# Kernel tuning notes

Hardware: AMD Instinct MI355X
Metric: run time of the kernel (lower is better)

## Reference

```python
import jax, jax.numpy as jnp
import numpy as np

B, L, H, S = 64, 1024, 768, 32
NH, HD = 8, H // 8
SEP = 102
EPS_LN = 1e-5


def setup_inputs() -> dict:
    key = jax.random.key(0)
    ks = jax.random.split(key, 16)
    # input_ids with exactly S SEP tokens per row at positions (j+1)*(L//S)-1
    ids = jax.random.randint(ks[0], (B, L), 1000, 30000, dtype=jnp.int64)
    sep_idx = (jnp.arange(1, S + 1) * (L // S)) - 1  # [S]
    ids = ids.at[:, sep_idx].set(SEP)
    attention_mask = jnp.ones((B, L), dtype=jnp.int32)
    labels = jax.random.randint(ks[1], (B, S), 0, 2, dtype=jnp.int64)
    sequence_output = jax.random.normal(ks[2], (B, L, H), dtype=jnp.float32)
    sc = 0.02
    params = dict(
        enc_W=jax.random.normal(ks[3], (H, H), jnp.float32) * sc,
        enc_b=jnp.zeros((H,), jnp.float32),
        enc_ln_g=jnp.ones((H,), jnp.float32),
        enc_ln_b=jnp.zeros((H,), jnp.float32),
        in_proj_W=jax.random.normal(ks[4], (3 * H, H), jnp.float32) * sc,
        in_proj_b=jnp.zeros((3 * H,), jnp.float32),
        out_proj_W=jax.random.normal(ks[5], (H, H), jnp.float32) * sc,
        out_proj_b=jnp.zeros((H,), jnp.float32),
        cls_W1=jax.random.normal(ks[6], (H, H), jnp.float32) * sc,
        cls_b1=jnp.zeros((H,), jnp.float32),
        cls_ln_g=jnp.ones((H,), jnp.float32),
        cls_ln_b=jnp.zeros((H,), jnp.float32),
        cls_W2=jax.random.normal(ks[7], (2, H), jnp.float32) * sc,
        cls_b2=jnp.zeros((2,), jnp.float32),
    )
    return dict(input_ids=ids, attention_mask=attention_mask, labels=labels,
                sequence_output=sequence_output, **params)


def _layernorm(x, g, b):
    m = jnp.mean(x, axis=-1, keepdims=True)
    v = jnp.mean((x - m) ** 2, axis=-1, keepdims=True)
    return (x - m) * jax.lax.rsqrt(v + EPS_LN) * g + b


def _gelu(x):
    return jax.nn.gelu(x, approximate=False)


def reference(input_ids, attention_mask, labels, sequence_output,
              enc_W, enc_b, enc_ln_g, enc_ln_b,
              in_proj_W, in_proj_b, out_proj_W, out_proj_b,
              cls_W1, cls_b1, cls_ln_g, cls_ln_b, cls_W2, cls_b2):
    # sep positions per sample (exactly S per row by construction)
    sep_pos = jax.vmap(lambda r: jnp.nonzero(r == SEP, size=S, fill_value=L - 1)[0])(input_ids)  # [B,S]
    all_pos = jnp.concatenate([jnp.zeros((B, 1), sep_pos.dtype), sep_pos], axis=1)  # [B,S+1]
    starts, ends = all_pos[:, :S], all_pos[:, 1:]  # inclusive [start, end] as in slice start:end+1
    t = jnp.arange(L)
    seg = (t[None, None, :] >= starts[:, :, None]) & (t[None, None, :] <= ends[:, :, None])  # [B,S,L]
    m = seg.astype(jnp.float32) * attention_mask[:, None, :].astype(jnp.float32)
    denom = jnp.sum(m, axis=-1, keepdims=True) + 1e-10  # [B,S,1]
    reps = jnp.einsum('bsl,bld->bsd', m, sequence_output) / denom  # segment mean pool
    # sentence encoder: Linear -> LN -> (dropout off) -> GELU
    x = _gelu(_layernorm(reps @ enc_W.T + enc_b, enc_ln_g, enc_ln_b))  # [B,S,H]
    # per-sample MHA (self-attention over sentences), dropout off
    qkv = x @ in_proj_W.T + in_proj_b  # [B,S,3H]
    q, k, v = jnp.split(qkv, 3, axis=-1)
    def heads(z):
        return z.reshape(B, S, NH, HD).transpose(0, 2, 1, 3)  # [B,NH,S,HD]
    q, k, v = heads(q), heads(k), heads(v)
    scores = jnp.einsum('bhqd,bhkd->bhqk', q, k) / jnp.sqrt(jnp.float32(HD))
    attn = jax.nn.softmax(scores, axis=-1)
    o = jnp.einsum('bhqk,bhkd->bhqd', attn, v).transpose(0, 2, 1, 3).reshape(B, S, H)
    attended = o @ out_proj_W.T + out_proj_b
    # classifier
    h = _gelu(_layernorm(attended @ cls_W1.T + cls_b1, cls_ln_g, cls_ln_b))
    logits = h @ cls_W2.T + cls_b2  # [B,S,2] (current_sentences == max_sentences, no padding)
    # cross entropy with ignore_index=-100
    flat_logits = logits.reshape(-1, 2)
    flat_labels = labels.reshape(-1)
    valid = flat_labels != -100
    safe = jnp.where(valid, flat_labels, 0)
    logp = jax.nn.log_softmax(flat_logits, axis=-1)
    nll = -jnp.take_along_axis(logp, safe[:, None], axis=-1)[:, 0]
    loss = jnp.sum(jnp.where(valid, nll, 0.0)) / jnp.maximum(jnp.sum(valid), 1)
    return loss, logits
```

## Files before the change

kernel.cpp:

```cpp
#include <hip/hip_runtime.h>
#include <math.h>

#define Bdim 64
#define Ldim 1024
#define Hdim 768
#define Sdim 32
#define NHdim 8
#define HDdim 96
#define SEP_ID 102

typedef unsigned short ushort_t;
typedef __attribute__((ext_vector_type(8))) short bf16x8;
typedef __attribute__((ext_vector_type(4))) float f32x4;

__device__ __forceinline__ ushort_t f2b(float f) {
    unsigned u = __builtin_bit_cast(unsigned, f);
    u += 0x7fffu + ((u >> 16) & 1u);
    return (ushort_t)(u >> 16);
}
__device__ __forceinline__ float b2f(ushort_t v) {
    unsigned u = ((unsigned)v) << 16;
    return __builtin_bit_cast(float, u);
}

__global__ __launch_bounds__(1024) void prep_kernel(const int* __restrict__ ids,
                                                    int* __restrict__ sep_pos,
                                                    const float* __restrict__ w0,
                                                    const float* __restrict__ w1,
                                                    const float* __restrict__ w2,
                                                    const float* __restrict__ w3,
                                                    ushort_t* __restrict__ dst) {
    __shared__ unsigned long long masks[16];
    int blk = blockIdx.x;
    int t = threadIdx.x;
    if (blk < 64) {
        unsigned long long m = __ballot(ids[(size_t)blk * Ldim + t] == SEP_ID);
        if ((t & 63) == 0) masks[t >> 6] = m;
        __syncthreads();
        if (t == 0) {
            int cnt = 0;
            for (int w = 0; w < 16 && cnt < Sdim; ++w) {
                unsigned long long mk = masks[w];
                while (mk && cnt < Sdim) {
                    int bit = __ffsll((unsigned long long)mk) - 1;
                    sep_pos[blk * Sdim + cnt++] = w * 64 + bit;
                    mk &= mk - 1;
                }
            }
            for (; cnt < Sdim; ++cnt) sep_pos[blk * Sdim + cnt] = Ldim - 1;
        }
    } else {
        int idx = (blk - 64) * 1024 + t;
        const float* src; int off;
        if (idx < 147456)      { src = w0; off = idx; }
        else if (idx < 589824) { src = w1; off = idx - 147456; }
        else if (idx < 737280) { src = w2; off = idx - 589824; }
        else                   { src = w3; off = idx - 737280; }
        float4 v = ((const float4*)src)[off];
        ushort4 ov; ov.x = f2b(v.x); ov.y = f2b(v.y); ov.z = f2b(v.z); ov.w = f2b(v.w);
        ((ushort4*)dst)[idx] = ov;
    }
}

__global__ __launch_bounds__(192) void pool_kernel(const float* __restrict__ seq,
                                                   const int* __restrict__ sep_pos,
                                                   const int* __restrict__ amask,
                                                   ushort_t* __restrict__ reps) {
    int bs = blockIdx.x;
    int b = bs >> 5, s = bs & 31;
    int start = (s == 0) ? 0 : sep_pos[b * Sdim + s - 1];
    int end = sep_pos[b * Sdim + s];
    int t = threadIdx.x;
    const float* base = seq + (size_t)b * Ldim * Hdim;
    const int* am = amask + b * Ldim;
    float4 A0 = {0,0,0,0}, A1 = {0,0,0,0}, A2 = {0,0,0,0}, A3 = {0,0,0,0};
    float d0 = 0.f, d1 = 0.f, d2 = 0.f, d3 = 0.f;
    int l = start;
    for (; l + 3 <= end; l += 4) {
        float m0 = (float)am[l],     m1 = (float)am[l + 1];
        float m2 = (float)am[l + 2], m3 = (float)am[l + 3];
        float4 v0 = ((const float4*)(base + (size_t)l * Hdim))[t];
        float4 v1 = ((const float4*)(base + (size_t)(l + 1) * Hdim))[t];
        float4 v2 = ((const float4*)(base + (size_t)(l + 2) * Hdim))[t];
        float4 v3 = ((const float4*)(base + (size_t)(l + 3) * Hdim))[t];
        d0 += m0; d1 += m1; d2 += m2; d3 += m3;
        A0.x += m0 * v0.x; A0.y += m0 * v0.y; A0.z += m0 * v0.z; A0.w += m0 * v0.w;
        A1.x += m1 * v1.x; A1.y += m1 * v1.y; A1.z += m1 * v1.z; A1.w += m1 * v1.w;
        A2.x += m2 * v2.x; A2.y += m2 * v2.y; A2.z += m2 * v2.z; A2.w += m2 * v2.w;
        A3.x += m3 * v3.x; A3.y += m3 * v3.y; A3.z += m3 * v3.z; A3.w += m3 * v3.w;
    }
    for (; l <= end; ++l) {
        float m0 = (float)am[l];
        float4 v0 = ((const float4*)(base + (size_t)l * Hdim))[t];
        d0 += m0;
        A0.x += m0 * v0.x; A0.y += m0 * v0.y; A0.z += m0 * v0.z; A0.w += m0 * v0.w;
    }
    float denom = d0 + d1 + d2 + d3;
    float inv = 1.f / (denom + 1e-10f);
    float4 acc;
    acc.x = (A0.x + A1.x + A2.x + A3.x) * inv;
    acc.y = (A0.y + A1.y + A2.y + A3.y) * inv;
    acc.z = (A0.z + A1.z + A2.z + A3.z) * inv;
    acc.w = (A0.w + A1.w + A2.w + A3.w) * inv;
    ushort4 o;
    o.x = f2b(acc.x); o.y = f2b(acc.y); o.z = f2b(acc.z); o.w = f2b(acc.w);
    ((ushort4*)(reps + (size_t)bs * Hdim))[t] = o;
}

__global__ __launch_bounds__(256) void gemm_mfma(const ushort_t* __restrict__ A,
                                                 const ushort_t* __restrict__ W,
                                                 const float* __restrict__ bias,
                                                 ushort_t* __restrict__ Cout,
                                                 int M, int N, int K) {
    __shared__ __attribute__((aligned(16))) ushort_t Al[2][64][64];
    __shared__ __attribute__((aligned(16))) ushort_t Bl[2][64][64];
    int tid = threadIdx.x;
    int wid = tid >> 6, lane = tid & 63;
    int rowBase = blockIdx.x * 64, colBase = blockIdx.y * 64;
    int wm = (wid >> 1) * 32, wn = (wid & 1) * 32;

    int srow = lane >> 3;
    int sblk = (lane & 7) ^ srow;
    const ushort_t* Abase = A + (size_t)(rowBase + wid * 16 + srow) * K + sblk * 8;
    const ushort_t* Wbase = W + (size_t)(colBase + wid * 16 + srow) * K + sblk * 8;

    f32x4 acc[2][2] = {};

#define STAGE(bufi, kofs)                                                                    \
    do {                                                                                     \
        const ushort_t* ag = Abase + (kofs);                                                 \
        const ushort_t* wg = Wbase + (kofs);                                                 \
        __builtin_amdgcn_global_load_lds(ag,           &Al[bufi][wid * 16][0],     16, 0, 0); \
        __builtin_amdgcn_global_load_lds(ag + 8 * K,   &Al[bufi][wid * 16 + 8][0], 16, 0, 0); \
        __builtin_amdgcn_global_load_lds(wg,           &Bl[bufi][wid * 16][0],     16, 0, 0); \
        __builtin_amdgcn_global_load_lds(wg + 8 * K,   &Bl[bufi][wid * 16 + 8][0], 16, 0, 0); \
    } while (0)

    STAGE(0, 0);
    __syncthreads();
    int nk = K >> 6;
    int lr = lane & 15;
    int lxor = lane & 7;
    for (int t = 0; t < nk; ++t) {
        if (t + 1 < nk) STAGE((t + 1) & 1, (t + 1) * 64);
        int cb = t & 1;
#pragma unroll
        for (int ks = 0; ks < 2; ++ks) {
            int pblk = ((ks * 4 + (lane >> 4)) ^ lxor) * 8;
            bf16x8 af[2], wf[2];
            af[0] = *(const bf16x8*)&Al[cb][wm + lr][pblk];
            af[1] = *(const bf16x8*)&Al[cb][wm + 16 + lr][pblk];
            wf[0] = *(const bf16x8*)&Bl[cb][wn + lr][pblk];
            wf[1] = *(const bf16x8*)&Bl[cb][wn + 16 + lr][pblk];
#pragma unroll
            for (int i = 0; i < 2; ++i)
#pragma unroll
                for (int j = 0; j < 2; ++j)
                    acc[i][j] = __builtin_amdgcn_mfma_f32_16x16x32_bf16(af[i], wf[j], acc[i][j], 0, 0, 0);
        }
        __syncthreads();
    }
#undef STAGE

    int lrow = (lane >> 4) * 4, lcol = lane & 15;
#pragma unroll
    for (int ni = 0; ni < 2; ++ni) {
        int c = colBase + wn + ni * 16 + lcol;
        float bv = bias[c];
#pragma unroll
        for (int mi = 0; mi < 2; ++mi) {
            int rb = rowBase + wm + mi * 16 + lrow;
#pragma unroll
            for (int j = 0; j < 4; ++j)
                Cout[(size_t)(rb + j) * N + c] = f2b(acc[mi][ni][j] + bv);
        }
    }
}

__global__ __launch_bounds__(192) void ln_gelu(const ushort_t* __restrict__ X,
                                               const float* __restrict__ g,
                                               const float* __restrict__ bt,
                                               ushort_t* __restrict__ Y) {
    int row = blockIdx.x;
    int t = threadIdx.x;
    ushort4 v = ((const ushort4*)(X + (size_t)row * Hdim))[t];
    float vals[4] = { b2f(v.x), b2f(v.y), b2f(v.z), b2f(v.w) };
    float s = vals[0] + vals[1] + vals[2] + vals[3];
    float s2 = vals[0]*vals[0] + vals[1]*vals[1] + vals[2]*vals[2] + vals[3]*vals[3];
#pragma unroll
    for (int off = 32; off; off >>= 1) { s += __shfl_down(s, off); s2 += __shfl_down(s2, off); }
    __shared__ float red[6];
    int wid = t >> 6;
    if ((t & 63) == 0) { red[wid * 2] = s; red[wid * 2 + 1] = s2; }
    __syncthreads();
    s  = red[0] + red[2] + red[4];
    s2 = red[1] + red[3] + red[5];
    float mean = s / Hdim;
    float var  = s2 / Hdim - mean * mean;
    float rstd = rsqrtf(var + 1e-5f);
    float4 gv = ((const float4*)g)[t];
    float4 bv = ((const float4*)bt)[t];
    float gg[4] = { gv.x, gv.y, gv.z, gv.w };
    float bb[4] = { bv.x, bv.y, bv.z, bv.w };
    ushort4 o;
    ushort_t* op = (ushort_t*)&o;
#pragma unroll
    for (int i = 0; i < 4; ++i) {
        float xn = (vals[i] - mean) * rstd * gg[i] + bb[i];
        float ge = 0.5f * xn * (1.f + erff(xn * 0.70710678118654752f));
        op[i] = f2b(ge);
    }
    ((ushort4*)(Y + (size_t)row * Hdim))[t] = o;
}

__global__ __launch_bounds__(256) void attn_kernel(const ushort_t* __restrict__ qkv,
                                                   ushort_t* __restrict__ o) {
    int bh = blockIdx.x;
    int b = bh >> 3, h = bh & 7;
    __shared__ float qs[Sdim][100], ks_[Sdim][100], vs[Sdim][100];
    __shared__ float sc[Sdim][33];
    int tid = threadIdx.x;
    for (int idx = tid; idx < 2304; idx += 256) {
        int m = idx / 768;
        int w = idx - m * 768;
        int s = w / 24, d4 = (w - s * 24) * 4;
        ushort4 v = *(const ushort4*)(qkv + (size_t)(b * Sdim + s) * (3 * Hdim) + m * Hdim + h * HDdim + d4);
        float* dst = (m == 0 ? &qs[s][d4] : (m == 1 ? &ks_[s][d4] : &vs[s][d4]));
        dst[0] = b2f(v.x); dst[1] = b2f(v.y); dst[2] = b2f(v.z); dst[3] = b2f(v.w);
    }
    __syncthreads();
    int ti = tid >> 4, tj = tid & 15;
    float a00 = 0.f, a01 = 0.f, a10 = 0.f, a11 = 0.f;
#pragma unroll 6
    for (int d = 0; d < HDdim; d += 4) {
        float4 q0 = *(const float4*)&qs[ti][d];
        float4 q1 = *(const float4*)&qs[ti + 16][d];
        float4 k0 = *(const float4*)&ks_[tj][d];
        float4 k1 = *(const float4*)&ks_[tj + 16][d];
        a00 += q0.x*k0.x + q0.y*k0.y + q0.z*k0.z + q0.w*k0.w;
        a01 += q0.x*k1.x + q0.y*k1.y + q0.z*k1.z + q0.w*k1.w;
        a10 += q1.x*k0.x + q1.y*k0.y + q1.z*k0.z + q1.w*k0.w;
        a11 += q1.x*k1.x + q1.y*k1.y + q1.z*k1.z + q1.w*k1.w;
    }
    const float sscale = 0.102062072615966f;
    sc[ti][tj]           = a00 * sscale;
    sc[ti][tj + 16]      = a01 * sscale;
    sc[ti + 16][tj]      = a10 * sscale;
    sc[ti + 16][tj + 16] = a11 * sscale;
    __syncthreads();
    int row = tid >> 3, jg = tid & 7;
    float v0 = sc[row][jg], v1 = sc[row][jg + 8], v2 = sc[row][jg + 16], v3 = sc[row][jg + 24];
    float mx = fmaxf(fmaxf(v0, v1), fmaxf(v2, v3));
#pragma unroll
    for (int m = 1; m <= 4; m <<= 1) mx = fmaxf(mx, __shfl_xor(mx, m));
    v0 = expf(v0 - mx); v1 = expf(v1 - mx); v2 = expf(v2 - mx); v3 = expf(v3 - mx);
    float sum = v0 + v1 + v2 + v3;
#pragma unroll
    for (int m = 1; m <= 4; m <<= 1) sum += __shfl_xor(sum, m);
    float inv = 1.f / sum;
    sc[row][jg] = v0 * inv; sc[row][jg + 8] = v1 * inv;
    sc[row][jg + 16] = v2 * inv; sc[row][jg + 24] = v3 * inv;
    __syncthreads();
    for (int idx = tid; idx < 768; idx += 256) {
        int ii = idx / 24, d4 = (idx - ii * 24) * 4;
        float o0 = 0.f, o1 = 0.f, o2 = 0.f, o3 = 0.f;
#pragma unroll 8
        for (int j = 0; j < Sdim; ++j) {
            float p = sc[ii][j];
            float4 vv = *(const float4*)&vs[j][d4];
            o0 += p * vv.x; o1 += p * vv.y; o2 += p * vv.z; o3 += p * vv.w;
        }
        ushort4 ov; ov.x = f2b(o0); ov.y = f2b(o1); ov.z = f2b(o2); ov.w = f2b(o3);
        *(ushort4*)(o + (size_t)(b * Sdim + ii) * Hdim + h * HDdim + d4) = ov;
    }
}

__global__ __launch_bounds__(192) void logits_kernel(const ushort_t* __restrict__ Hh,
                                                     const float* __restrict__ W2,
                                                     const float* __restrict__ b2,
                                                     float* __restrict__ out) {
    int row = blockIdx.x;
    int t = threadIdx.x;
    ushort4 hv = ((const ushort4*)(Hh + (size_t)row * Hdim))[t];
    float4 w0 = ((const float4*)W2)[t];
    float4 w1 = ((const float4*)(W2 + Hdim))[t];
    float h0 = b2f(hv.x), h1 = b2f(hv.y), h2 = b2f(hv.z), h3 = b2f(hv.w);
    float a0 = h0 * w0.x + h1 * w0.y + h2 * w0.z + h3 * w0.w;
    float a1 = h0 * w1.x + h1 * w1.y + h2 * w1.z + h3 * w1.w;
#pragma unroll
    for (int off = 32; off; off >>= 1) { a0 += __shfl_down(a0, off); a1 += __shfl_down(a1, off); }
    __shared__ float red[6];
    int wid = t >> 6;
    if ((t & 63) == 0) { red[wid * 2] = a0; red[wid * 2 + 1] = a1; }
    __syncthreads();
    if (t == 0) {
        out[row * 2 + 0] = red[0] + red[2] + red[4] + b2[0];
        out[row * 2 + 1] = red[1] + red[3] + red[5] + b2[1];
    }
}

__global__ __launch_bounds__(256) void loss_kernel(const float* __restrict__ logits,
                                                   const int* __restrict__ labels,
                                                   float* __restrict__ out) {
    int t = threadIdx.x;
    float sum = 0.f, cnt = 0.f;
    for (int i = t; i < Bdim * Sdim; i += 256) {
        int lab = labels[i];
        if (lab != -100) {
            float l0 = logits[i * 2], l1 = logits[i * 2 + 1];
            float mx = fmaxf(l0, l1);
            float lse = mx + logf(expf(l0 - mx) + expf(l1 - mx));
            sum += lse - (lab ? l1 : l0);
            cnt += 1.f;
        }
    }
#pragma unroll
    for (int off = 32; off; off >>= 1) { sum += __shfl_down(sum, off); cnt += __shfl_down(cnt, off); }
    __shared__ float red[8];
    int wid = t >> 6;
    if ((t & 63) == 0) { red[wid * 2] = sum; red[wid * 2 + 1] = cnt; }
    __syncthreads();
    if (t == 0) {
        float ts = red[0] + red[2] + red[4] + red[6];
        float tc = red[1] + red[3] + red[5] + red[7];
        out[0] = ts / fmaxf(tc, 1.f);
    }
}

extern "C" void kernel_launch(void* const* d_in, const int* in_sizes, int n_in,
                              void* d_out, int out_size, void* d_ws, size_t ws_size,
                              hipStream_t stream) {
    const int*   input_ids  = (const int*)d_in[0];
    const int*   amask      = (const int*)d_in[1];
    const int*   labels     = (const int*)d_in[2];
    const float* seq        = (const float*)d_in[3];
    const float* enc_W      = (const float*)d_in[4];
    const float* enc_b      = (const float*)d_in[5];
    const float* enc_ln_g   = (const float*)d_in[6];
    const float* enc_ln_b   = (const float*)d_in[7];
    const float* in_proj_W  = (const float*)d_in[8];
    const float* in_proj_b  = (const float*)d_in[9];
    const float* out_proj_W = (const float*)d_in[10];
    const float* out_proj_b = (const float*)d_in[11];
    const float* cls_W1     = (const float*)d_in[12];
    const float* cls_b1     = (const float*)d_in[13];
    const float* cls_ln_g   = (const float*)d_in[14];
    const float* cls_ln_b   = (const float*)d_in[15];
    const float* cls_W2     = (const float*)d_in[16];
    const float* cls_b2     = (const float*)d_in[17];

    float* out = (float*)d_out;

    char* ws = (char*)d_ws;
    const size_t MS = (size_t)Bdim * Sdim;
    int*      sep_pos = (int*)ws;
    ushort_t* wbf     = (ushort_t*)(ws + 8192);
    ushort_t* bf_a    = (ushort_t*)(ws + 8192 + 7077888);
    ushort_t* bf_b    = bf_a + MS * Hdim;
    ushort_t* bf_c    = bf_b + MS * Hdim;
    ushort_t* bf_d    = bf_c + MS * Hdim;
    ushort_t* bf_qkv  = bf_d + MS * Hdim;

    ushort_t* encWb     = wbf;
    ushort_t* inprojWb  = wbf + 589824;
    ushort_t* outprojWb = wbf + 2359296;
    ushort_t* clsW1b    = wbf + 2949120;

    prep_kernel<<<928, 1024, 0, stream>>>(input_ids, sep_pos,
                                          enc_W, in_proj_W, out_proj_W, cls_W1, wbf);
    pool_kernel<<<Bdim * Sdim, 192, 0, stream>>>(seq, sep_pos, amask, bf_a);
    { dim3 g(32, 12); gemm_mfma<<<g, 256, 0, stream>>>(bf_a, encWb, enc_b, bf_d, (int)MS, Hdim, Hdim); }
    ln_gelu<<<Bdim * Sdim, 192, 0, stream>>>(bf_d, enc_ln_g, enc_ln_b, bf_b);
    { dim3 g(32, 36); gemm_mfma<<<g, 256, 0, stream>>>(bf_b, inprojWb, in_proj_b, bf_qkv, (int)MS, 3 * Hdim, Hdim); }
    attn_kernel<<<Bdim * NHdim, 256, 0, stream>>>(bf_qkv, bf_c);
    { dim3 g(32, 12); gemm_mfma<<<g, 256, 0, stream>>>(bf_c, outprojWb, out_proj_b, bf_a, (int)MS, Hdim, Hdim); }
    { dim3 g(32, 12); gemm_mfma<<<g, 256, 0, stream>>>(bf_a, clsW1b, cls_b1, bf_d, (int)MS, Hdim, Hdim); }
    ln_gelu<<<Bdim * Sdim, 192, 0, stream>>>(bf_d, cls_ln_g, cls_ln_b, bf_b);
    logits_kernel<<<Bdim * Sdim, 192, 0, stream>>>(bf_b, cls_W2, cls_b2, out + 1);
    loss_kernel<<<1, 256, 0, stream>>>(out + 1, labels, out);
}
```

Measured before the change: 120.8 us.

## Fuse SEP scan into pooling kernel and fuse classifier LN-GELU into logits

Merges the prep and pool kernels: each pooling block recomputes its own SEP positions from a ballot scan of its row, and the weight bf16 conversion blocks share the same launch. Separately, fuses the final layernorm+GELU with the 2-way logits projection, so the intermediate bf16 activation is no longer written and re-read. This removes two launches and a global sep_pos round trip. The cost is redundant SEP scanning (32 blocks per row) and a one-pass variance formula with slightly different numerics.

```diff
diff --git a/kernel.cpp b/kernel.cpp
--- a/kernel.cpp
+++ b/kernel.cpp
@@ -23,34 +23,19 @@
     return __builtin_bit_cast(float, u);
 }
 
-__global__ __launch_bounds__(1024) void prep_kernel(const int* __restrict__ ids,
-                                                    int* __restrict__ sep_pos,
-                                                    const float* __restrict__ w0,
-                                                    const float* __restrict__ w1,
-                                                    const float* __restrict__ w2,
-                                                    const float* __restrict__ w3,
-                                                    ushort_t* __restrict__ dst) {
-    __shared__ unsigned long long masks[16];
+__global__ __launch_bounds__(192) void prep_pool_kernel(const float* __restrict__ seq,
+                                                        const int* __restrict__ ids,
+                                                        const int* __restrict__ amask,
+                                                        const float* __restrict__ w0,
+                                                        const float* __restrict__ w1,
+                                                        const float* __restrict__ w2,
+                                                        const float* __restrict__ w3,
+                                                        ushort_t* __restrict__ wdst,
+                                                        ushort_t* __restrict__ reps) {
     int blk = blockIdx.x;
     int t = threadIdx.x;
-    if (blk < 64) {
-        unsigned long long m = __ballot(ids[(size_t)blk * Ldim + t] == SEP_ID);
-        if ((t & 63) == 0) masks[t >> 6] = m;
-        __syncthreads();
-        if (t == 0) {
-            int cnt = 0;
-            for (int w = 0; w < 16 && cnt < Sdim; ++w) {
-                unsigned long long mk = masks[w];
-                while (mk && cnt < Sdim) {
-                    int bit = __ffsll((unsigned long long)mk) - 1;
-                    sep_pos[blk * Sdim + cnt++] = w * 64 + bit;
-                    mk &= mk - 1;
-                }
-            }
-            for (; cnt < Sdim; ++cnt) sep_pos[blk * Sdim + cnt] = Ldim - 1;
-        }
-    } else {
-        int idx = (blk - 64) * 1024 + t;
+    if (blk >= 2048) {
+        int idx = (blk - 2048) * 192 + t;
         const float* src; int off;
         if (idx < 147456)      { src = w0; off = idx; }
         else if (idx < 589824) { src = w1; off = idx - 147456; }
@@ -58,19 +43,46 @@
         else                   { src = w3; off = idx - 737280; }
         float4 v = ((const float4*)src)[off];
         ushort4 ov; ov.x = f2b(v.x); ov.y = f2b(v.y); ov.z = f2b(v.z); ov.w = f2b(v.w);
-        ((ushort4*)dst)[idx] = ov;
-    }
-}
-
-__global__ __launch_bounds__(192) void pool_kernel(const float* __restrict__ seq,
-                                                   const int* __restrict__ sep_pos,
-                                                   const int* __restrict__ amask,
-                                                   ushort_t* __restrict__ reps) {
-    int bs = blockIdx.x;
-    int b = bs >> 5, s = bs & 31;
-    int start = (s == 0) ? 0 : sep_pos[b * Sdim + s - 1];
-    int end = sep_pos[b * Sdim + s];
-    int t = threadIdx.x;
+        ((ushort4*)wdst)[idx] = ov;
+        return;
+    }
+    int b = blk >> 5, s = blk & 31;
+    __shared__ unsigned long long masks[18];
+    const int* idrow = ids + (size_t)b * Ldim;
+    int wv = t >> 6, ln = t & 63;
+#pragma unroll
+    for (int r = 0; r < 6; ++r) {
+        int p = r * 192 + t;
+        bool is = (p < Ldim) && (idrow[p] == SEP_ID);
+        unsigned long long m = __ballot(is);
+        if (ln == 0) masks[r * 3 + wv] = m;
+    }
+    __syncthreads();
+    int start, end;
+    {
+        int need0 = s - 1, need1 = s;
+        int p0 = Ldim - 1, p1 = Ldim - 1;
+        int cnt = 0;
+#pragma unroll
+        for (int i = 0; i < 18; ++i) {
+            unsigned long long mk = masks[i];
+            int pc = __popcll(mk);
+            int base = (i / 3) * 192 + (i % 3) * 64;
+            if (need0 >= cnt && need0 < cnt + pc) {
+                unsigned long long mm = mk;
+                for (int j = cnt; j < need0; ++j) mm &= mm - 1;
+                p0 = base + __ffsll(mm) - 1;
+            }
+            if (need1 >= cnt && need1 < cnt + pc) {
+                unsigned long long mm = mk;
+                for (int j = cnt; j < need1; ++j) mm &= mm - 1;
+                p1 = base + __ffsll(mm) - 1;
+            }
+            cnt += pc;
+        }
+        start = (s == 0) ? 0 : p0;
+        end = p1;
+    }
     const float* base = seq + (size_t)b * Ldim * Hdim;
     const int* am = amask + b * Ldim;
     float4 A0 = {0,0,0,0}, A1 = {0,0,0,0}, A2 = {0,0,0,0}, A3 = {0,0,0,0};
@@ -104,7 +116,7 @@
     acc.w = (A0.w + A1.w + A2.w + A3.w) * inv;
     ushort4 o;
     o.x = f2b(acc.x); o.y = f2b(acc.y); o.z = f2b(acc.z); o.w = f2b(acc.w);
-    ((ushort4*)(reps + (size_t)bs * Hdim))[t] = o;
+    ((ushort4*)(reps + (size_t)blk * Hdim))[t] = o;
 }
 
 __global__ __launch_bounds__(256) void gemm_mfma(const ushort_t* __restrict__ A,
@@ -275,27 +287,52 @@
     }
 }
 
-__global__ __launch_bounds__(192) void logits_kernel(const ushort_t* __restrict__ Hh,
-                                                     const float* __restrict__ W2,
-                                                     const float* __restrict__ b2,
-                                                     float* __restrict__ out) {
+__global__ __launch_bounds__(192) void cls_head_kernel(const ushort_t* __restrict__ X,
+                                                       const float* __restrict__ g,
+                                                       const float* __restrict__ bt,
+                                                       const float* __restrict__ W2,
+                                                       const float* __restrict__ b2,
+                                                       float* __restrict__ out) {
     int row = blockIdx.x;
     int t = threadIdx.x;
-    ushort4 hv = ((const ushort4*)(Hh + (size_t)row * Hdim))[t];
+    ushort4 v = ((const ushort4*)(X + (size_t)row * Hdim))[t];
+    float vals[4] = { b2f(v.x), b2f(v.y), b2f(v.z), b2f(v.w) };
+    float s = vals[0] + vals[1] + vals[2] + vals[3];
+    float s2 = vals[0]*vals[0] + vals[1]*vals[1] + vals[2]*vals[2] + vals[3]*vals[3];
+#pragma unroll
+    for (int off = 32; off; off >>= 1) { s += __shfl_down(s, off); s2 += __shfl_down(s2, off); }
+    __shared__ float red1[6], red2[6];
+    int wid = t >> 6;
+    if ((t & 63) == 0) { red1[wid * 2] = s; red1[wid * 2 + 1] = s2; }
+    __syncthreads();
+    s  = red1[0] + red1[2] + red1[4];
+    s2 = red1[1] + red1[3] + red1[5];
+    float mean = s / Hdim;
+    float var  = s2 / Hdim - mean * mean;
+    float rstd = rsqrtf(var + 1e-5f);
+    float4 gv = ((const float4*)g)[t];
+    float4 bv = ((const float4*)bt)[t];
     float4 w0 = ((const float4*)W2)[t];
     float4 w1 = ((const float4*)(W2 + Hdim))[t];
-    float h0 = b2f(hv.x), h1 = b2f(hv.y), h2 = b2f(hv.z), h3 = b2f(hv.w);
-    float a0 = h0 * w0.x + h1 * w0.y + h2 * w0.z + h3 * w0.w;
-    float a1 = h0 * w1.x + h1 * w1.y + h2 * w1.z + h3 * w1.w;
+    float gg[4] = { gv.x, gv.y, gv.z, gv.w };
+    float bb[4] = { bv.x, bv.y, bv.z, bv.w };
+    float ww0[4] = { w0.x, w0.y, w0.z, w0.w };
+    float ww1[4] = { w1.x, w1.y, w1.z, w1.w };
+    float a0 = 0.f, a1 = 0.f;
+#pragma unroll
+    for (int i = 0; i < 4; ++i) {
+        float xn = (vals[i] - mean) * rstd * gg[i] + bb[i];
+        float ge = 0.5f * xn * (1.f + erff(xn * 0.70710678118654752f));
+        a0 += ge * ww0[i];
+        a1 += ge * ww1[i];
+    }
 #pragma unroll
     for (int off = 32; off; off >>= 1) { a0 += __shfl_down(a0, off); a1 += __shfl_down(a1, off); }
-    __shared__ float red[6];
-    int wid = t >> 6;
-    if ((t & 63) == 0) { red[wid * 2] = a0; red[wid * 2 + 1] = a1; }
+    if ((t & 63) == 0) { red2[wid * 2] = a0; red2[wid * 2 + 1] = a1; }
     __syncthreads();
     if (t == 0) {
-        out[row * 2 + 0] = red[0] + red[2] + red[4] + b2[0];
-        out[row * 2 + 1] = red[1] + red[3] + red[5] + b2[1];
+        out[row * 2 + 0] = red2[0] + red2[2] + red2[4] + b2[0];
+        out[row * 2 + 1] = red2[1] + red2[3] + red2[5] + b2[1];
     }
 }
 
@@ -353,9 +390,8 @@
 
     char* ws = (char*)d_ws;
     const size_t MS = (size_t)Bdim * Sdim;
-    int*      sep_pos = (int*)ws;
-    ushort_t* wbf     = (ushort_t*)(ws + 8192);
-    ushort_t* bf_a    = (ushort_t*)(ws + 8192 + 7077888);
+    ushort_t* wbf     = (ushort_t*)(ws);
+    ushort_t* bf_a    = (ushort_t*)(ws + 7077888);
     ushort_t* bf_b    = bf_a + MS * Hdim;
     ushort_t* bf_c    = bf_b + MS * Hdim;
     ushort_t* bf_d    = bf_c + MS * Hdim;
@@ -366,16 +402,15 @@
     ushort_t* outprojWb = wbf + 2359296;
     ushort_t* clsW1b    = wbf + 2949120;
 
-    prep_kernel<<<928, 1024, 0, stream>>>(input_ids, sep_pos,
-                                          enc_W, in_proj_W, out_proj_W, cls_W1, wbf);
-    pool_kernel<<<Bdim * Sdim, 192, 0, stream>>>(seq, sep_pos, amask, bf_a);
+    prep_pool_kernel<<<6656, 192, 0, stream>>>(seq, input_ids, amask,
+                                               enc_W, in_proj_W, out_proj_W, cls_W1,
+                                               wbf, bf_a);
     { dim3 g(32, 12); gemm_mfma<<<g, 256, 0, stream>>>(bf_a, encWb, enc_b, bf_d, (int)MS, Hdim, Hdim); }
     ln_gelu<<<Bdim * Sdim, 192, 0, stream>>>(bf_d, enc_ln_g, enc_ln_b, bf_b);
     { dim3 g(32, 36); gemm_mfma<<<g, 256, 0, stream>>>(bf_b, inprojWb, in_proj_b, bf_qkv, (int)MS, 3 * Hdim, Hdim); }
     attn_kernel<<<Bdim * NHdim, 256, 0, stream>>>(bf_qkv, bf_c);
     { dim3 g(32, 12); gemm_mfma<<<g, 256, 0, stream>>>(bf_c, outprojWb, out_proj_b, bf_a, (int)MS, Hdim, Hdim); }
     { dim3 g(32, 12); gemm_mfma<<<g, 256, 0, stream>>>(bf_a, clsW1b, cls_b1, bf_d, (int)MS, Hdim, Hdim); }
-    ln_gelu<<<Bdim * Sdim, 192, 0, stream>>>(bf_d, cls_ln_g, cls_ln_b, bf_b);
-    logits_kernel<<<Bdim * Sdim, 192, 0, stream>>>(bf_b, cls_W2, cls_b2, out + 1);
+    cls_head_kernel<<<Bdim * Sdim, 192, 0, stream>>>(bf_d, cls_ln_g, cls_ln_b, cls_W2, cls_b2, out + 1);
     loss_kernel<<<1, 256, 0, stream>>>(out + 1, labels, out);
 }
```

After: 117.7 us. -2.6%, faster.
